# Performance work log

Measured on AMD Instinct MI355X. Metric: run time of the kernel, lower is better.

The kernel has to match this reference:

```python
import jax, jax.numpy as jnp
import numpy as np

N_NODES = 62      # config.note_num (SEED EEG electrodes)
BATCH   = 1024    # graphs per batch
IN_CH   = 5
HID     = 64
OUT_CH  = 3
K_HOPS  = 2       # config.K


def setup_inputs() -> dict:
    key = jax.random.key(0)
    ks = jax.random.split(key, 8)
    total = BATCH * N_NODES
    x = jax.random.normal(ks[0], (total, IN_CH), dtype=jnp.float32)
    # fully-connected per-graph edge_index in row-major order (incl. self-loops),
    # matching edge_weight.reshape(-1).repeat(batch_size) in the torch code
    src = jnp.repeat(jnp.arange(N_NODES, dtype=jnp.int32), N_NODES)
    dst = jnp.tile(jnp.arange(N_NODES, dtype=jnp.int32), N_NODES)
    offs = (jnp.arange(BATCH, dtype=jnp.int32) * N_NODES)[:, None]
    edge_index = jnp.stack([
        (src[None, :] + offs).reshape(-1),
        (dst[None, :] + offs).reshape(-1),
    ])  # [2, BATCH*3844]
    batch = jnp.repeat(jnp.arange(BATCH, dtype=jnp.int32), N_NODES)
    n_tril = N_NODES * (N_NODES + 1) // 2  # 1953
    edge_weight_param = jax.random.normal(ks[1], (n_tril,), dtype=jnp.float32)
    w1 = jax.random.normal(ks[2], (HID, IN_CH), dtype=jnp.float32) * (1.0 / np.sqrt(IN_CH))
    b1 = jnp.zeros((HID,), dtype=jnp.float32)
    w2 = jax.random.normal(ks[3], (HID, HID), dtype=jnp.float32) * (1.0 / np.sqrt(HID))
    b2 = jnp.zeros((HID,), dtype=jnp.float32)
    wfc = jax.random.normal(ks[4], (OUT_CH, HID), dtype=jnp.float32) * (1.0 / np.sqrt(HID))
    bfc = jnp.zeros((OUT_CH,), dtype=jnp.float32)
    return dict(x=x, edge_index=edge_index, batch=batch,
                edge_weight_param=edge_weight_param,
                w1=w1, b1=b1, w2=w2, b2=b2, wfc=wfc, bfc=bfc)


def _gcn_norm(edge_index, edge_weight, num_nodes):
    # Graph already contains every self-loop, so add_remaining_self_loops only
    # reorders edges; normalization math is identical on the original edge set.
    row, col = edge_index[0], edge_index[1]
    deg = jax.ops.segment_sum(jnp.abs(edge_weight), row, num_segments=num_nodes)
    deg_inv_sqrt = jnp.where(deg > 0, jax.lax.rsqrt(deg), 0.0)
    return deg_inv_sqrt[row] * edge_weight * deg_inv_sqrt[col]


def _rsgconv(x, src, dst, norm, w, b):
    n = x.shape[0]
    for _ in range(K_HOPS):  # K propagation hops (gather-scale-scatter)
        x = jax.ops.segment_sum(norm[:, None] * x[src], dst, num_segments=n)
    return x @ w.T + b


def reference(x, edge_index, batch, edge_weight_param, w1, b1, w2, b2, wfc, bfc):
    num_nodes = x.shape[0]
    # rebuild symmetric dense 62x62 edge-weight matrix from learnable tril vector
    xs, ys = jnp.tril_indices(N_NODES)
    W = jnp.zeros((N_NODES, N_NODES), dtype=x.dtype).at[xs, ys].set(edge_weight_param)
    W = W + W.T - jnp.diag(jnp.diag(W))
    edge_weight = jnp.tile(W.reshape(-1), BATCH)  # [BATCH*3844]
    norm = _gcn_norm(edge_index, edge_weight, num_nodes)
    src, dst = edge_index[0], edge_index[1]
    h = jax.nn.relu(_rsgconv(x, src, dst, norm, w1, b1))
    h = jax.nn.relu(_rsgconv(h, src, dst, norm, w2, b2))
    pooled = jax.ops.segment_sum(h, batch, num_segments=BATCH)  # global_add_pool
    # dropout is identity in eval mode
    return pooled @ wfc.T + bfc
```

## Files before the change

### kernel.cpp

```cpp
#include <hip/hip_runtime.h>

#define NN 62
#define NP 64
#define NBATCH 1024
#define IN_CH 5
#define HID 64
#define OUT_CH 3
#define NTRIL 1953
#define H1S 72
#define GS 17

typedef _Float16 f16;
typedef f16 half8 __attribute__((ext_vector_type(8)));
typedef float floatx4 __attribute__((ext_vector_type(4)));

__global__ __launch_bounds__(64) void setup_k(const float* __restrict__ p,
                                              const float* __restrict__ w2,
                                              float* __restrict__ A2g,
                                              f16* __restrict__ a2h,
                                              f16* __restrict__ a2l,
                                              f16* __restrict__ w2h,
                                              f16* __restrict__ w2l) {
    __shared__ float sA[NN * NP];
    __shared__ float sDinv[NN];
    const int lane = threadIdx.x;
    const int n = blockIdx.x;

    {
        float wv = w2[n * HID + lane];
        f16 wh = (f16)wv;
        w2h[n * NP + lane] = wh;
        w2l[n * NP + lane] = (f16)(wv - (float)wh);
    }

    for (int i = lane; i < NN * NP; i += 64) sA[i] = 0.f;
    __syncthreads();

    for (int i = lane; i < NTRIL; i += 64) {
        int r = (int)((sqrtf(8.f * (float)i + 1.f) - 1.f) * 0.5f);
        while (r * (r + 1) / 2 > i) --r;
        while ((r + 1) * (r + 2) / 2 <= i) ++r;
        int c = i - r * (r + 1) / 2;
        float v = p[i];
        sA[r * NP + c] = v;
        sA[c * NP + r] = v;
    }
    __syncthreads();

    if (lane < NN) {
        float s = 0.f;
        for (int j = 0; j < NN; ++j) s += fabsf(sA[lane * NP + j]);
        sDinv[lane] = (s > 0.f) ? (1.0f / sqrtf(s)) : 0.f;
    }
    __syncthreads();

    for (int i = lane; i < NN * NP; i += 64) {
        int r = i >> 6, c = i & 63;
        float dc = (c < NN) ? sDinv[c] : 0.f;
        sA[i] = sDinv[r] * sA[i] * dc;
    }
    __syncthreads();

    float acc = 0.f;
    if (n < NN)
        for (int k = 0; k < NN; ++k) acc += sA[n * NP + k] * sA[k * NP + lane];
    A2g[n * NP + lane] = acc;
    f16 ah = (f16)acc;
    a2h[n * NP + lane] = ah;
    a2l[n * NP + lane] = (f16)(acc - (float)ah);
}

__global__ __launch_bounds__(256, 4) void graph_net(
    const float* __restrict__ x, const float* __restrict__ A2g,
    const f16* __restrict__ a2h, const f16* __restrict__ a2l,
    const f16* __restrict__ w2h, const f16* __restrict__ w2l,
    const float* __restrict__ w1, const float* __restrict__ b1,
    const float* __restrict__ b2,
    const float* __restrict__ wfc, const float* __restrict__ bfc,
    float* __restrict__ out) {
    __shared__ float sY1[NP * 8];
    __shared__ f16 sH1h[NP * H1S];
    __shared__ f16 sH1l[NP * H1S];
    __shared__ float sG[4 * NP * GS];
    __shared__ float sPool[NP];

    const int t = threadIdx.x;
    const int lane = t & 63;
    const int w = __builtin_amdgcn_readfirstlane(t >> 6);
    const int g = blockIdx.x;
    const float* xg = x + (size_t)g * (NN * IN_CH);

    {
        const int n = t >> 2;
        const int q = t & 3;
        float y0 = 0.f, y1v = 0.f, y2 = 0.f, y3 = 0.f, y4 = 0.f;
        if (n < NN) {
#pragma unroll
            for (int j = 0; j < 16; ++j) {
                int k = q + 4 * j;
                if (k < NN) {
                    float a = A2g[n * NP + k];
                    const float* xr = xg + k * IN_CH;
                    y0 += a * xr[0]; y1v += a * xr[1]; y2 += a * xr[2];
                    y3 += a * xr[3]; y4 += a * xr[4];
                }
            }
        }
        y0 += __shfl_xor(y0, 1); y0 += __shfl_xor(y0, 2);
        y1v += __shfl_xor(y1v, 1); y1v += __shfl_xor(y1v, 2);
        y2 += __shfl_xor(y2, 1); y2 += __shfl_xor(y2, 2);
        y3 += __shfl_xor(y3, 1); y3 += __shfl_xor(y3, 2);
        y4 += __shfl_xor(y4, 1); y4 += __shfl_xor(y4, 2);
        if (q == 0 && n < NN) {
            float4 v; v.x = y0; v.y = y1v; v.z = y2; v.w = y3;
            *(float4*)(sY1 + n * 8) = v;
            sY1[n * 8 + 4] = y4;
        }
    }
    __syncthreads();

    {
        const float* wr = w1 + lane * IN_CH;
        float q0 = wr[0], q1 = wr[1], q2 = wr[2], q3 = wr[3], q4 = wr[4];
        float bb = b1[lane];
#pragma unroll
        for (int ni = 0; ni < 16; ++ni) {
            const int n = 16 * w + ni;
            if (n < NN) {
                float4 yv = *(const float4*)(sY1 + n * 8);
                float y4v = sY1[n * 8 + 4];
                float h = bb + yv.x * q0 + yv.y * q1 + yv.z * q2
                             + yv.w * q3 + y4v * q4;
                h = fmaxf(h, 0.f);
                f16 hh = (f16)h;
                sH1h[n * H1S + lane] = hh;
                sH1l[n * H1S + lane] = (f16)(h - (float)hh);
            }
        }
    }
    if (t < 128) {
        const int n = 62 + (t >> 6);
        sH1h[n * H1S + (t & 63)] = (f16)0.f;
        sH1l[n * H1S + (t & 63)] = (f16)0.f;
    }
    __syncthreads();

    const int jn = lane & 15;
    const int qd = lane >> 4;
    const int jglob = 16 * w + jn;

    half8 bWh[2], bWl[2];
#pragma unroll
    for (int ks = 0; ks < 2; ++ks) {
        bWh[ks] = *(const half8*)(w2h + jglob * NP + qd * 8 + 32 * ks);
        bWl[ks] = *(const half8*)(w2l + jglob * NP + qd * 8 + 32 * ks);
    }
    floatx4 Cg[4];
#pragma unroll
    for (int T = 0; T < 4; ++T) { Cg[T][0]=0.f; Cg[T][1]=0.f; Cg[T][2]=0.f; Cg[T][3]=0.f; }
#pragma unroll
    for (int T = 0; T < 4; ++T) {
#pragma unroll
        for (int ks = 0; ks < 2; ++ks) {
            const half8 aH = *(const half8*)(sH1h + (16 * T + jn) * H1S + qd * 8 + 32 * ks);
            const half8 aL = *(const half8*)(sH1l + (16 * T + jn) * H1S + qd * 8 + 32 * ks);
            Cg[T] = __builtin_amdgcn_mfma_f32_16x16x32_f16(aL, bWh[ks], Cg[T], 0, 0, 0);
            Cg[T] = __builtin_amdgcn_mfma_f32_16x16x32_f16(aH, bWl[ks], Cg[T], 0, 0, 0);
            Cg[T] = __builtin_amdgcn_mfma_f32_16x16x32_f16(aH, bWh[ks], Cg[T], 0, 0, 0);
        }
    }
    {
        float* gw = sG + w * (NP * GS);
#pragma unroll
        for (int T = 0; T < 4; ++T)
#pragma unroll
            for (int r = 0; r < 4; ++r)
                gw[(16 * T + qd * 4 + r) * GS + jn] = Cg[T][r];
    }
    __syncthreads();

    half8 bGh[2], bGl[2];
    {
        const float* gw = sG + w * (NP * GS);
#pragma unroll
        for (int ks = 0; ks < 2; ++ks) {
#pragma unroll
            for (int i = 0; i < 8; ++i) {
                float v = gw[(qd * 8 + i + 32 * ks) * GS + jn];
                f16 vh = (f16)v;
                bGh[ks][i] = vh;
                bGl[ks][i] = (f16)(v - (float)vh);
            }
        }
    }

    floatx4 C2[4];
#pragma unroll
    for (int T = 0; T < 4; ++T) { C2[T][0]=0.f; C2[T][1]=0.f; C2[T][2]=0.f; C2[T][3]=0.f; }
#pragma unroll
    for (int T = 0; T < 4; ++T) {
#pragma unroll
        for (int ks = 0; ks < 2; ++ks) {
            const half8 aH = *(const half8*)(a2h + (16 * T + jn) * NP + qd * 8 + 32 * ks);
            const half8 aL = *(const half8*)(a2l + (16 * T + jn) * NP + qd * 8 + 32 * ks);
            C2[T] = __builtin_amdgcn_mfma_f32_16x16x32_f16(aL, bGh[ks], C2[T], 0, 0, 0);
            C2[T] = __builtin_amdgcn_mfma_f32_16x16x32_f16(aH, bGl[ks], C2[T], 0, 0, 0);
            C2[T] = __builtin_amdgcn_mfma_f32_16x16x32_f16(aH, bGh[ks], C2[T], 0, 0, 0);
        }
    }

    {
        const float b2r = b2[jglob];
        float pool = 0.f;
#pragma unroll
        for (int T = 0; T < 4; ++T) {
#pragma unroll
            for (int r = 0; r < 4; ++r) {
                int n = 16 * T + qd * 4 + r;
                float v = fmaxf(C2[T][r] + b2r, 0.f);
                pool += (n < NN) ? v : 0.f;
            }
        }
        pool += __shfl_xor(pool, 16);
        pool += __shfl_xor(pool, 32);
        if (lane < 16) sPool[16 * w + lane] = pool;
    }
    __syncthreads();

    if (t < OUT_CH) {
        float v = bfc[t];
        const float* wr = wfc + t * HID;
#pragma unroll
        for (int h = 0; h < HID; ++h) v += sPool[h] * wr[h];
        out[g * OUT_CH + t] = v;
    }
}

extern "C" void kernel_launch(void* const* d_in, const int* in_sizes, int n_in,
                              void* d_out, int out_size, void* d_ws, size_t ws_size,
                              hipStream_t stream) {
    const float* x   = (const float*)d_in[0];
    const float* ewp = (const float*)d_in[3];
    const float* w1  = (const float*)d_in[4];
    const float* b1  = (const float*)d_in[5];
    const float* w2  = (const float*)d_in[6];
    const float* b2  = (const float*)d_in[7];
    const float* wfc = (const float*)d_in[8];
    const float* bfc = (const float*)d_in[9];
    float* out = (float*)d_out;

    float* A2g = (float*)d_ws;
    f16* a2h = (f16*)(A2g + NP * NP);
    f16* a2l = a2h + NP * NP;
    f16* w2h = a2l + NP * NP;
    f16* w2l = w2h + NP * NP;

    setup_k<<<NP, 64, 0, stream>>>(ewp, w2, A2g, a2h, a2l, w2h, w2l);
    graph_net<<<NBATCH, 256, 0, stream>>>(x, A2g, a2h, a2l, w2h, w2l,
                                          w1, b1, b2, wfc, bfc, out);
}
```

Measured before the change: 127.0 us.

## Reorder layer-1 as A2·(X·W1ᵀ) on MFMA and keep A2 fragments in registers

Layer 1 used to compute A2·X with scalar FMAs reading fp32 A2 from global memory, then apply W1. It now computes U = X·W1ᵀ first, with x values broadcast by readlane, and runs A2·U on split-fp16 MFMA. The A2 hi/lo fragments are loaded once into registers and reused for both layers' propagation GEMMs. Shared memory is aliased into one buffer, and the fp32 A2 workspace is dropped. This trades scalar global loads for more MFMA work and higher register pressure, which could lower occupancy.

Result: faster. 123.3 us (-2.9%).

```diff
diff --git a/kernel.cpp b/kernel.cpp
--- a/kernel.cpp
+++ b/kernel.cpp
@@ -16,7 +16,6 @@
 
 __global__ __launch_bounds__(64) void setup_k(const float* __restrict__ p,
                                               const float* __restrict__ w2,
-                                              float* __restrict__ A2g,
                                               f16* __restrict__ a2h,
                                               f16* __restrict__ a2l,
                                               f16* __restrict__ w2h,
@@ -64,25 +63,26 @@
     float acc = 0.f;
     if (n < NN)
         for (int k = 0; k < NN; ++k) acc += sA[n * NP + k] * sA[k * NP + lane];
-    A2g[n * NP + lane] = acc;
     f16 ah = (f16)acc;
     a2h[n * NP + lane] = ah;
     a2l[n * NP + lane] = (f16)(acc - (float)ah);
 }
 
 __global__ __launch_bounds__(256, 4) void graph_net(
-    const float* __restrict__ x, const float* __restrict__ A2g,
+    const float* __restrict__ x,
     const f16* __restrict__ a2h, const f16* __restrict__ a2l,
     const f16* __restrict__ w2h, const f16* __restrict__ w2l,
     const float* __restrict__ w1, const float* __restrict__ b1,
     const float* __restrict__ b2,
     const float* __restrict__ wfc, const float* __restrict__ bfc,
     float* __restrict__ out) {
-    __shared__ float sY1[NP * 8];
-    __shared__ f16 sH1h[NP * H1S];
-    __shared__ f16 sH1l[NP * H1S];
-    __shared__ float sG[4 * NP * GS];
-    __shared__ float sPool[NP];
+    __shared__ __align__(16) char smem[37120];
+    f16* sUTh = (f16*)smem;
+    f16* sUTl = (f16*)(smem + 9216);
+    float* sG  = (float*)smem;
+    f16* sH1h = (f16*)(smem + 18432);
+    f16* sH1l = (f16*)(smem + 27648);
+    float* sPool = (float*)(smem + 36864);
 
     const int t = threadIdx.x;
     const int lane = t & 63;
@@ -90,64 +90,82 @@
     const int g = blockIdx.x;
     const float* xg = x + (size_t)g * (NN * IN_CH);
 
-    {
-        const int n = t >> 2;
-        const int q = t & 3;
-        float y0 = 0.f, y1v = 0.f, y2 = 0.f, y3 = 0.f, y4 = 0.f;
-        if (n < NN) {
-#pragma unroll
-            for (int j = 0; j < 16; ++j) {
-                int k = q + 4 * j;
-                if (k < NN) {
-                    float a = A2g[n * NP + k];
-                    const float* xr = xg + k * IN_CH;
-                    y0 += a * xr[0]; y1v += a * xr[1]; y2 += a * xr[2];
-                    y3 += a * xr[3]; y4 += a * xr[4];
-                }
-            }
-        }
-        y0 += __shfl_xor(y0, 1); y0 += __shfl_xor(y0, 2);
-        y1v += __shfl_xor(y1v, 1); y1v += __shfl_xor(y1v, 2);
-        y2 += __shfl_xor(y2, 1); y2 += __shfl_xor(y2, 2);
-        y3 += __shfl_xor(y3, 1); y3 += __shfl_xor(y3, 2);
-        y4 += __shfl_xor(y4, 1); y4 += __shfl_xor(y4, 2);
-        if (q == 0 && n < NN) {
-            float4 v; v.x = y0; v.y = y1v; v.z = y2; v.w = y3;
-            *(float4*)(sY1 + n * 8) = v;
-            sY1[n * 8 + 4] = y4;
-        }
-    }
-    __syncthreads();
-
-    {
-        const float* wr = w1 + lane * IN_CH;
-        float q0 = wr[0], q1 = wr[1], q2 = wr[2], q3 = wr[3], q4 = wr[4];
-        float bb = b1[lane];
-#pragma unroll
-        for (int ni = 0; ni < 16; ++ni) {
-            const int n = 16 * w + ni;
-            if (n < NN) {
-                float4 yv = *(const float4*)(sY1 + n * 8);
-                float y4v = sY1[n * 8 + 4];
-                float h = bb + yv.x * q0 + yv.y * q1 + yv.z * q2
-                             + yv.w * q3 + y4v * q4;
-                h = fmaxf(h, 0.f);
-                f16 hh = (f16)h;
-                sH1h[n * H1S + lane] = hh;
-                sH1l[n * H1S + lane] = (f16)(h - (float)hh);
-            }
-        }
-    }
-    if (t < 128) {
-        const int n = 62 + (t >> 6);
-        sH1h[n * H1S + (t & 63)] = (f16)0.f;
-        sH1l[n * H1S + (t & 63)] = (f16)0.f;
-    }
-    __syncthreads();
-
     const int jn = lane & 15;
     const int qd = lane >> 4;
     const int jglob = 16 * w + jn;
+
+    half8 aFh[4][2], aFl[4][2];
+#pragma unroll
+    for (int T = 0; T < 4; ++T)
+#pragma unroll
+        for (int ks = 0; ks < 2; ++ks) {
+            aFh[T][ks] = *(const half8*)(a2h + (16 * T + jn) * NP + qd * 8 + 32 * ks);
+            aFl[T][ks] = *(const half8*)(a2l + (16 * T + jn) * NP + qd * 8 + 32 * ks);
+        }
+
+    int xi[IN_CH];
+    {
+        const int L = (lane < NN) ? lane : (NN - 1);
+        const int* xgi = (const int*)xg;
+#pragma unroll
+        for (int c = 0; c < IN_CH; ++c) xi[c] = xgi[L * IN_CH + c];
+    }
+    float w1r[IN_CH];
+#pragma unroll
+    for (int c = 0; c < IN_CH; ++c) w1r[c] = w1[lane * IN_CH + c];
+
+#pragma unroll
+    for (int ni = 0; ni < 16; ++ni) {
+        const int n = 16 * w + ni;
+        if (n < NN) {
+            float u = 0.f;
+#pragma unroll
+            for (int c = 0; c < IN_CH; ++c)
+                u += __int_as_float(__builtin_amdgcn_readlane(xi[c], n)) * w1r[c];
+            f16 uh = (f16)u;
+            sUTh[lane * H1S + n] = uh;
+            sUTl[lane * H1S + n] = (f16)(u - (float)uh);
+        }
+    }
+    if (t < 128) {
+        const int n = 62 + (t >> 6);
+        sUTh[(t & 63) * H1S + n] = (f16)0.f;
+        sUTl[(t & 63) * H1S + n] = (f16)0.f;
+    }
+    __syncthreads();
+
+    half8 bUh[2], bUl[2];
+#pragma unroll
+    for (int ks = 0; ks < 2; ++ks) {
+        bUh[ks] = *(const half8*)(sUTh + jglob * H1S + qd * 8 + 32 * ks);
+        bUl[ks] = *(const half8*)(sUTl + jglob * H1S + qd * 8 + 32 * ks);
+    }
+    floatx4 C1[4];
+#pragma unroll
+    for (int T = 0; T < 4; ++T) { C1[T][0]=0.f; C1[T][1]=0.f; C1[T][2]=0.f; C1[T][3]=0.f; }
+#pragma unroll
+    for (int T = 0; T < 4; ++T) {
+#pragma unroll
+        for (int ks = 0; ks < 2; ++ks) {
+            C1[T] = __builtin_amdgcn_mfma_f32_16x16x32_f16(aFl[T][ks], bUh[ks], C1[T], 0, 0, 0);
+            C1[T] = __builtin_amdgcn_mfma_f32_16x16x32_f16(aFh[T][ks], bUl[ks], C1[T], 0, 0, 0);
+            C1[T] = __builtin_amdgcn_mfma_f32_16x16x32_f16(aFh[T][ks], bUh[ks], C1[T], 0, 0, 0);
+        }
+    }
+    {
+        const float b1r = b1[jglob];
+#pragma unroll
+        for (int T = 0; T < 4; ++T)
+#pragma unroll
+            for (int r = 0; r < 4; ++r) {
+                const int n = 16 * T + qd * 4 + r;
+                float v = fmaxf(C1[T][r] + b1r, 0.f);
+                f16 vh = (f16)v;
+                sH1h[n * H1S + jglob] = vh;
+                sH1l[n * H1S + jglob] = (f16)(v - (float)vh);
+            }
+    }
+    __syncthreads();
 
     half8 bWh[2], bWl[2];
 #pragma unroll
@@ -181,17 +199,16 @@
 
     half8 bGh[2], bGl[2];
     {
-        const float* gw = sG + w * (NP * GS);
-#pragma unroll
-        for (int ks = 0; ks < 2; ++ks) {
+        const float* gr = sG + w * (NP * GS);
+#pragma unroll
+        for (int ks = 0; ks < 2; ++ks)
 #pragma unroll
             for (int i = 0; i < 8; ++i) {
-                float v = gw[(qd * 8 + i + 32 * ks) * GS + jn];
+                float v = gr[(qd * 8 + i + 32 * ks) * GS + jn];
                 f16 vh = (f16)v;
                 bGh[ks][i] = vh;
                 bGl[ks][i] = (f16)(v - (float)vh);
             }
-        }
     }
 
     floatx4 C2[4];
@@ -201,11 +218,9 @@
     for (int T = 0; T < 4; ++T) {
 #pragma unroll
         for (int ks = 0; ks < 2; ++ks) {
-            const half8 aH = *(const half8*)(a2h + (16 * T + jn) * NP + qd * 8 + 32 * ks);
-            const half8 aL = *(const half8*)(a2l + (16 * T + jn) * NP + qd * 8 + 32 * ks);
-            C2[T] = __builtin_amdgcn_mfma_f32_16x16x32_f16(aL, bGh[ks], C2[T], 0, 0, 0);
-            C2[T] = __builtin_amdgcn_mfma_f32_16x16x32_f16(aH, bGl[ks], C2[T], 0, 0, 0);
-            C2[T] = __builtin_amdgcn_mfma_f32_16x16x32_f16(aH, bGh[ks], C2[T], 0, 0, 0);
+            C2[T] = __builtin_amdgcn_mfma_f32_16x16x32_f16(aFl[T][ks], bGh[ks], C2[T], 0, 0, 0);
+            C2[T] = __builtin_amdgcn_mfma_f32_16x16x32_f16(aFh[T][ks], bGl[ks], C2[T], 0, 0, 0);
+            C2[T] = __builtin_amdgcn_mfma_f32_16x16x32_f16(aFh[T][ks], bGh[ks], C2[T], 0, 0, 0);
         }
     }
 
@@ -213,17 +228,16 @@
         const float b2r = b2[jglob];
         float pool = 0.f;
 #pragma unroll
-        for (int T = 0; T < 4; ++T) {
+        for (int T = 0; T < 4; ++T)
 #pragma unroll
             for (int r = 0; r < 4; ++r) {
-                int n = 16 * T + qd * 4 + r;
+                const int n = 16 * T + qd * 4 + r;
                 float v = fmaxf(C2[T][r] + b2r, 0.f);
                 pool += (n < NN) ? v : 0.f;
             }
-        }
         pool += __shfl_xor(pool, 16);
         pool += __shfl_xor(pool, 32);
-        if (lane < 16) sPool[16 * w + lane] = pool;
+        if (lane < 16) sPool[jglob] = pool;
     }
     __syncthreads();
 
@@ -231,7 +245,7 @@
         float v = bfc[t];
         const float* wr = wfc + t * HID;
 #pragma unroll
-        for (int h = 0; h < HID; ++h) v += sPool[h] * wr[h];
+        for (int m = 0; m < HID; ++m) v += sPool[m] * wr[m];
         out[g * OUT_CH + t] = v;
     }
 }
@@ -249,13 +263,12 @@
     const float* bfc = (const float*)d_in[9];
     float* out = (float*)d_out;
 
-    float* A2g = (float*)d_ws;
-    f16* a2h = (f16*)(A2g + NP * NP);
+    f16* a2h = (f16*)d_ws;
     f16* a2l = a2h + NP * NP;
     f16* w2h = a2l + NP * NP;
     f16* w2l = w2h + NP * NP;
 
-    setup_k<<<NP, 64, 0, stream>>>(ewp, w2, A2g, a2h, a2l, w2h, w2l);
-    graph_net<<<NBATCH, 256, 0, stream>>>(x, A2g, a2h, a2l, w2h, w2l,
+    setup_k<<<NP, 64, 0, stream>>>(ewp, w2, a2h, a2l, w2h, w2l);
+    graph_net<<<NBATCH, 256, 0, stream>>>(x, a2h, a2l, w2h, w2l,
                                           w1, b1, b2, wfc, bfc, out);
 }
```
